# Kernel tuning notes

Measured on AMD Instinct MI355X. Metric: run time of the kernel, lower is better.

## Reference

```python
import jax, jax.numpy as jnp
import numpy as np

D = 1280      # embed_dim
H = 20        # num_heads
HD = D // H   # head_dim = 64
B = 4         # batch (number of requests)
ENC = 1500    # encoder length per request (Whisper 30s)
KV = B * ENC  # 6000 packed cross kv tokens
SEQ = [300, 500, 350, 450]  # ragged decoder lengths, sum = 1600
Q = sum(SEQ)


def setup_inputs() -> dict:
    key = jax.random.key(0)
    ks = jax.random.split(key, 8)
    s = 0.02
    return {
        "hidden_states": jax.random.normal(ks[0], (Q, D), jnp.float32),
        "cross_hidden_states": jax.random.normal(ks[1], (KV, D), jnp.float32),
        "seq_lens": jnp.array(SEQ, dtype=jnp.int32),
        "Wq": jax.random.normal(ks[2], (D, D), jnp.float32) * s,
        "bq": jax.random.normal(ks[3], (D,), jnp.float32) * s,
        "Wkv": jax.random.normal(ks[4], (D, 2 * D), jnp.float32) * s,
        "bkv": jax.random.normal(ks[5], (2 * D,), jnp.float32) * s,
        "Wo": jax.random.normal(ks[6], (D, D), jnp.float32) * s,
        "bo": jax.random.normal(ks[7], (D,), jnp.float32) * s,
    }


def reference(hidden_states, cross_hidden_states, seq_lens, Wq, bq, Wkv, bkv, Wo, bo):
    q_len, d = hidden_states.shape
    kv_len = cross_hidden_states.shape[0]
    bsz = seq_lens.shape[0]
    enc_len = kv_len // bsz
    scaling = jnp.float32(HD) ** -0.5

    # projections (packed tokens)
    q = (hidden_states @ Wq + bq) * scaling           # [Q, D]
    kv = cross_hidden_states @ Wkv + bkv              # [KV, 2D]
    k, v = kv[:, :d], kv[:, d:]

    # [H, L, HD]
    qh = q.reshape(q_len, H, HD).transpose(1, 0, 2)
    kh = k.reshape(kv_len, H, HD).transpose(1, 0, 2)
    vh = v.reshape(kv_len, H, HD).transpose(1, 0, 2)

    scores = jnp.einsum("hqd,hkd->hqk", qh, kh)       # [H, Q, KV]

    # ragged block-diagonal mask: query token i belongs to request
    # searchsorted(cumsum(seq_lens), i, 'right'); kv token j to j // enc_len
    cum = jnp.cumsum(seq_lens)
    q_req = jnp.searchsorted(cum, jnp.arange(q_len), side="right")
    kv_req = jnp.arange(kv_len) // enc_len
    mask = q_req[:, None] == kv_req[None, :]          # [Q, KV] bool

    scores = jnp.where(mask[None, :, :], scores, -jnp.inf)
    probs = jax.nn.softmax(scores, axis=-1)
    attn = jnp.einsum("hqk,hkd->hqd", probs, vh)      # [H, Q, HD]
    attn = attn.transpose(1, 0, 2).reshape(q_len, d)
    return attn @ Wo + bo
```

## Files before the change

kernel.cpp:

```cpp
#include <hip/hip_runtime.h>
#include <stdint.h>

#define AS1 __attribute__((address_space(1)))
#define AS3 __attribute__((address_space(3)))

typedef __bf16 bf16_t;
typedef bf16_t bf16x8 __attribute__((ext_vector_type(8)));
typedef float  f32x4  __attribute__((ext_vector_type(4)));
typedef float  f32x16 __attribute__((ext_vector_type(16)));
typedef unsigned short u16;

constexpr int D     = 1280;
constexpr int H     = 20;
constexpr int HD    = 64;
constexpr int NQ    = 1600;
constexpr int NKV   = 6000;
constexpr int ENC   = 1500;
constexpr int QPAD  = 1632;
constexpr int KVP   = 1504;
constexpr int KVTOT = 4 * KVP;
constexpr int KB_PER_REQ = KVP / 32;
constexpr int KB_TOT     = 4 * KB_PER_REQ;

__device__ __forceinline__ u16 f2bf(float f) {
  union { float f; uint32_t u; } x; x.f = f;
  uint32_t r = (x.u + 0x7fffu + ((x.u >> 16) & 1u)) >> 16;
  return (u16)r;
}

__device__ __forceinline__ void gload16(const void* g, void* l) {
  __builtin_amdgcn_global_load_lds((AS1 void*)g, (AS3 void*)l, 16, 0, 0);
}

__device__ __forceinline__ void cvt_body(const float* __restrict__ in, u16* __restrict__ out,
                                         int i, int n4) {
  if (i >= n4) return;
  float4 v = ((const float4*)in)[i];
  ushort4 o;
  o.x = f2bf(v.x); o.y = f2bf(v.y); o.z = f2bf(v.z); o.w = f2bf(v.w);
  ((ushort4*)out)[i] = o;
}

__device__ __forceinline__ void tpose_body(const float* __restrict__ in, u16* __restrict__ out,
                                           int R, int C, int bx, int by, u16 (*tile)[33]) {
  int bc = bx * 32, br = by * 32;
  int tx = threadIdx.x & 31, ty = threadIdx.x >> 5;
#pragma unroll
  for (int i = 0; i < 32; i += 8)
    tile[ty + i][tx] = f2bf(in[(size_t)(br + ty + i) * C + bc + tx]);
  __syncthreads();
#pragma unroll
  for (int i = 0; i < 32; i += 8)
    out[(size_t)(bc + ty + i) * R + br + tx] = tile[tx][ty + i];
}

__global__ __launch_bounds__(256)
void prep_kernel(const float* __restrict__ hs, const float* __restrict__ chs,
                 const float* __restrict__ Wq, const float* __restrict__ Wkv,
                 const float* __restrict__ Wo,
                 u16* __restrict__ hsb, u16* __restrict__ chsb,
                 u16* __restrict__ Wqt, u16* __restrict__ Wkvt, u16* __restrict__ Wot) {
  __shared__ u16 tile[32][33];
  int b = blockIdx.x;
  if (b < 2000) {
    cvt_body(hs, hsb, b * 256 + threadIdx.x, 512000);
  } else if (b < 9500) {
    cvt_body(chs, chsb, (b - 2000) * 256 + threadIdx.x, 1920000);
  } else if (b < 11100) {
    int t = b - 9500;  tpose_body(Wq,  Wqt,  1280, 1280, t % 40, t / 40, tile);
  } else if (b < 14300) {
    int t = b - 11100; tpose_body(Wkv, Wkvt, 1280, 2560, t % 80, t / 80, tile);
  } else {
    int t = b - 14300; tpose_body(Wo,  Wot,  1280, 1280, t % 40, t / 40, tile);
  }
}

template <int MODE>
__device__ __forceinline__ void gemm_tile(
    int m0, int n0, const u16* __restrict__ A, const u16* __restrict__ Bt,
    const float* __restrict__ bias, int M,
    u16* __restrict__ outA, u16* __restrict__ outB, float* __restrict__ outF,
    u16* As, u16* Bs) {
  const int tid = threadIdx.x;
  const int lane = tid & 63, l15 = lane & 15, lg = lane >> 4;
  const int w = tid >> 6, wr = w >> 1, wc = w & 1;

  const bool vside = (MODE == 1) && (n0 >= D);

  f32x4 acc[4][4] = {};

  for (int k0 = 0; k0 < D; k0 += 64) {
#pragma unroll
    for (int p = 0; p < 4; ++p) {
      int off = p * 4096 + tid * 16;
      int lg_off = off ^ (((off >> 7) & 7) << 4);
      int row = lg_off >> 7, kb = lg_off & 127;
      int gr = m0 + row; gr = gr < M ? gr : M - 1;
      gload16((const char*)A + ((size_t)gr * D + k0) * 2 + kb, (char*)As + off);
    }
#pragma unroll
    for (int p = 0; p < 4; ++p) {
      int off = p * 4096 + tid * 16;
      int lg_off = off ^ (((off >> 7) & 7) << 4);
      int row = lg_off >> 7, kb = lg_off & 127;
      int gr = n0 + row;
      gload16((const char*)Bt + ((size_t)gr * D + k0) * 2 + kb, (char*)Bs + off);
    }
    __syncthreads();
#pragma unroll
    for (int kk = 0; kk < 2; ++kk) {
      const int kbyte = kk * 64 + lg * 16;
      bf16x8 af[4], bfr[4];
#pragma unroll
      for (int m = 0; m < 4; ++m) {
        int row = wr * 64 + m * 16 + l15;
        int addr = ((row << 7) + kbyte) ^ ((row & 7) << 4);
        af[m] = *(const bf16x8*)((const char*)As + addr);
      }
#pragma unroll
      for (int n = 0; n < 4; ++n) {
        int row = wc * 64 + n * 16 + l15;
        int addr = ((row << 7) + kbyte) ^ ((row & 7) << 4);
        bfr[n] = *(const bf16x8*)((const char*)Bs + addr);
      }
      if (!vside) {
#pragma unroll
        for (int m = 0; m < 4; ++m)
#pragma unroll
          for (int n = 0; n < 4; ++n)
            acc[m][n] = __builtin_amdgcn_mfma_f32_16x16x32_bf16(af[m], bfr[n], acc[m][n], 0, 0, 0);
      } else {
#pragma unroll
        for (int m = 0; m < 4; ++m)
#pragma unroll
          for (int n = 0; n < 4; ++n)
            acc[m][n] = __builtin_amdgcn_mfma_f32_16x16x32_bf16(bfr[n], af[m], acc[m][n], 0, 0, 0);
      }
    }
    __syncthreads();
  }

  if (!vside) {
#pragma unroll
    for (int m = 0; m < 4; ++m)
#pragma unroll
      for (int n = 0; n < 4; ++n) {
        int col = n0 + wc * 64 + n * 16 + l15;
        float bv = bias[col];
#pragma unroll
        for (int r = 0; r < 4; ++r) {
          int row = m0 + wr * 64 + m * 16 + lg * 4 + r;
          if (row >= M) continue;
          float v = acc[m][n][r] + bv;
          if (MODE == 0) {
            v *= 0.125f;
            int h = col >> 6, hd = col & 63;
            outA[((size_t)(h * QPAD + row)) * HD + hd] = f2bf(v);
          } else if (MODE == 1) {
            int req = row / ENC, loc = row - req * ENC;
            int rr = req * KVP + loc;
            int h = col >> 6, hd = col & 63;
            int kb2 = rr >> 5, kv = rr & 31;
            outA[((size_t)((h * KB_TOT + kb2) * 4 + (hd >> 4))) * 512 + kv * 16 + (hd & 15)] = f2bf(v);
          } else {
            outF[(size_t)row * D + col] = v;
          }
        }
      }
  } else {
    float bvv[4][4];
#pragma unroll
    for (int n = 0; n < 4; ++n)
#pragma unroll
      for (int r = 0; r < 4; ++r)
        bvv[n][r] = bias[n0 + wc * 64 + n * 16 + lg * 4 + r];
#pragma unroll
    for (int m = 0; m < 4; ++m) {
      int gm = m0 + wr * 64 + m * 16 + l15;
      int req = gm / ENC, loc = gm - req * ENC;
      int rr = req * KVP + loc;
      int kb2 = rr >> 5, kv = rr & 31;
      bool ok = gm < M;
#pragma unroll
      for (int n = 0; n < 4; ++n)
#pragma unroll
        for (int r = 0; r < 4; ++r) {
          if (!ok) continue;
          int c2 = n0 + wc * 64 + n * 16 + lg * 4 + r - D;
          int h = c2 >> 6, hd = c2 & 63;
          outB[((size_t)((h * KB_TOT + kb2) * 64 + hd)) * 32 + kv] = f2bf(acc[m][n][r] + bvv[n][r]);
        }
    }
  }
}

__global__ __launch_bounds__(256)
void qkv_gemm_kernel(const u16* __restrict__ hsb, const u16* __restrict__ chsb,
                     const u16* __restrict__ Wqt, const u16* __restrict__ Wkvt,
                     const float* __restrict__ bq, const float* __restrict__ bkv,
                     u16* __restrict__ qhb, u16* __restrict__ khb, u16* __restrict__ vtb) {
  __shared__ __align__(16) u16 As[128 * 64];
  __shared__ __align__(16) u16 Bs[128 * 64];
  const int nwg = 1070, q8 = nwg >> 3, r8 = nwg & 7;
  const int xcd = blockIdx.x & 7, pos = blockIdx.x >> 3;
  const int wg = (xcd < r8 ? xcd * (q8 + 1) : r8 * (q8 + 1) + (xcd - r8) * q8) + pos;
  if (wg < 940) {
    gemm_tile<1>((wg / 20) * 128, (wg % 20) * 128, chsb, Wkvt, bkv, NKV,
                 khb, vtb, nullptr, As, Bs);
  } else {
    int w2 = wg - 940;
    gemm_tile<0>((w2 / 10) * 128, (w2 % 10) * 128, hsb, Wqt, bq, NQ,
                 qhb, nullptr, nullptr, As, Bs);
  }
}

__global__ __launch_bounds__(256)
void o_gemm_kernel(const u16* __restrict__ attnb, const u16* __restrict__ Wot,
                   const float* __restrict__ bo, float* __restrict__ out) {
  __shared__ __align__(16) u16 As[128 * 64];
  __shared__ __align__(16) u16 Bs[128 * 64];
  const int nwg = 130, q8 = nwg >> 3, r8 = nwg & 7;
  const int xcd = blockIdx.x & 7, pos = blockIdx.x >> 3;
  const int wg = (xcd < r8 ? xcd * (q8 + 1) : r8 * (q8 + 1) + (xcd - r8) * q8) + pos;
  gemm_tile<2>((wg / 10) * 128, (wg % 10) * 128, attnb, Wot, bo, NQ,
               nullptr, nullptr, out, As, Bs);
}

__global__ __launch_bounds__(256)
void attn_kernel(const u16* __restrict__ kbuf, const u16* __restrict__ vbuf,
                 const u16* __restrict__ qh, const int* __restrict__ seq,
                 u16* __restrict__ attnb) {
  __shared__ __align__(16) float smem[4][2176];
  const int lane = threadIdx.x & 63;
  const int l31 = lane & 31, h5 = lane >> 5;
  const int w = threadIdx.x >> 6;

  const int xcd = blockIdx.x & 7, pos = blockIdx.x >> 3;
  const int g = xcd * 160 + pos;
  const int p = g >> 4, t = g & 15;
  const int head = p >> 2, req = p & 3;

  int s0 = seq[0], s1 = seq[1], s2 = seq[2];
  int qstart = (req > 0 ? s0 : 0) + (req > 1 ? s1 : 0) + (req > 2 ? s2 : 0);
  int slen = seq[req];
  int q0 = t * 32;
  if (q0 >= slen) return;

  const u16* qrow = qh + ((size_t)(head * QPAD + qstart + q0 + l31)) * HD + h5 * 8;
  bf16x8 qb[4];
#pragma unroll
  for (int ks = 0; ks < 4; ++ks) qb[ks] = *(const bf16x8*)(qrow + ks * 16);

  const u16* kpan = kbuf + (size_t)(head * KB_TOT + req * KB_PER_REQ) * 2048 + l31 * 16 + h5 * 8;
  const u16* vpan = vbuf + (size_t)(head * KB_TOT + req * KB_PER_REQ) * 2048 + l31 * 32 + h5 * 8;
  const float C = 1.44269504088896340736f;

  f32x16 o0 = {}, o1 = {};
  float mx = -__builtin_inff(), ls = 0.f;

  const int kvs = w * 384;
  const int kve = (w == 3) ? ENC : kvs + 384;

  bf16x8 ka[4], va[2][2], kan[4], van[2][2];
  {
    const u16* kp = kpan + (size_t)(kvs >> 5) * 2048;
    const u16* vp = vpan + (size_t)(kvs >> 5) * 2048;
#pragma unroll
    for (int ks = 0; ks < 4; ++ks) ka[ks] = *(const bf16x8*)(kp + ks * 512);
#pragma unroll
    for (int dt = 0; dt < 2; ++dt)
#pragma unroll
      for (int ks = 0; ks < 2; ++ks)
        va[dt][ks] = *(const bf16x8*)(vp + dt * 1024 + ks * 16);
  }

  for (int kvb = kvs; kvb < kve; kvb += 32) {
    int nb = (kvb + 32 < kve ? kvb + 32 : kvs) >> 5;
    {
      const u16* kp = kpan + (size_t)nb * 2048;
      const u16* vp = vpan + (size_t)nb * 2048;
#pragma unroll
      for (int ks = 0; ks < 4; ++ks) kan[ks] = *(const bf16x8*)(kp + ks * 512);
#pragma unroll
      for (int dt = 0; dt < 2; ++dt)
#pragma unroll
        for (int ks = 0; ks < 2; ++ks)
          van[dt][ks] = *(const bf16x8*)(vp + dt * 1024 + ks * 16);
    }

    f32x16 sa = {};
    __builtin_amdgcn_s_setprio(1);
#pragma unroll
    for (int ks = 0; ks < 4; ++ks)
      sa = __builtin_amdgcn_mfma_f32_32x32x16_bf16(ka[ks], qb[ks], sa, 0, 0, 0);
    __builtin_amdgcn_s_setprio(0);

    if (kvb + 32 > ENC) {
#pragma unroll
      for (int r = 0; r < 16; ++r) {
        int kvr = (r & 3) + 4 * h5 + 8 * (r >> 2);
        sa[r] = (kvb + kvr >= ENC) ? -__builtin_inff() : sa[r];
      }
    }

    float tm = sa[0];
#pragma unroll
    for (int r = 1; r < 16; ++r) tm = fmaxf(tm, sa[r]);
    tm = fmaxf(tm, __shfl_xor(tm, 32));

    if (__any(tm > mx + 8.0f)) {
      float mnew = fmaxf(mx, tm);
      float sc = exp2f((mx - mnew) * C);
      mx = mnew;
      ls *= sc;
      o0 *= sc; o1 *= sc;
    }
    float psum = 0.f;
#pragma unroll
    for (int r = 0; r < 16; ++r) { sa[r] = exp2f((sa[r] - mx) * C); psum += sa[r]; }
    ls += psum;

    uint32_t a[8], x[8];
#pragma unroll
    for (int i = 0; i < 8; ++i)
      a[i] = (uint32_t)f2bf(sa[2 * i]) | ((uint32_t)f2bf(sa[2 * i + 1]) << 16);
#pragma unroll
    for (int i = 0; i < 8; ++i) x[i] = (uint32_t)__shfl_xor((int)a[i], 32);
    union { uint32_t w4[4]; bf16x8 v; } pb0, pb1;
    pb0.w4[0] = h5 ? x[2] : a[0]; pb0.w4[1] = h5 ? x[3] : a[1];
    pb0.w4[2] = h5 ? a[2] : x[0]; pb0.w4[3] = h5 ? a[3] : x[1];
    pb1.w4[0] = h5 ? x[6] : a[4]; pb1.w4[1] = h5 ? x[7] : a[5];
    pb1.w4[2] = h5 ? a[6] : x[4]; pb1.w4[3] = h5 ? a[7] : x[5];

    __builtin_amdgcn_s_setprio(1);
    o0 = __builtin_amdgcn_mfma_f32_32x32x16_bf16(va[0][0], pb0.v, o0, 0, 0, 0);
    o0 = __builtin_amdgcn_mfma_f32_32x32x16_bf16(va[0][1], pb1.v, o0, 0, 0, 0);
    o1 = __builtin_amdgcn_mfma_f32_32x32x16_bf16(va[1][0], pb0.v, o1, 0, 0, 0);
    o1 = __builtin_amdgcn_mfma_f32_32x32x16_bf16(va[1][1], pb1.v, o1, 0, 0, 0);
    __builtin_amdgcn_s_setprio(0);

#pragma unroll
    for (int ks = 0; ks < 4; ++ks) ka[ks] = kan[ks];
#pragma unroll
    for (int dt = 0; dt < 2; ++dt)
#pragma unroll
      for (int ks = 0; ks < 2; ++ks) va[dt][ks] = van[dt][ks];
  }

  ls += __shfl_xor(ls, 32);

#pragma unroll
  for (int r = 0; r < 16; ++r) {
    int drow = (r & 3) + 8 * (r >> 2) + 4 * h5;
    smem[w][drow * 33 + l31] = o0[r];
    smem[w][(drow + 32) * 33 + l31] = o1[r];
  }
  if (h5 == 0) {
    smem[w][2112 + l31] = mx;
    smem[w][2144 + l31] = ls;
  }
  __syncthreads();

#pragma unroll
  for (int it = 0; it < 8; ++it) {
    int item = threadIdx.x + it * 256;
    int q = item >> 6, d = item & 63;
    float m0v = smem[0][2112 + q], m1v = smem[1][2112 + q];
    float m2v = smem[2][2112 + q], m3v = smem[3][2112 + q];
    float M = fmaxf(fmaxf(m0v, m1v), fmaxf(m2v, m3v));
    float e0 = exp2f((m0v - M) * C), e1 = exp2f((m1v - M) * C);
    float e2 = exp2f((m2v - M) * C), e3 = exp2f((m3v - M) * C);
    float L = smem[0][2144 + q] * e0 + smem[1][2144 + q] * e1 +
              smem[2][2144 + q] * e2 + smem[3][2144 + q] * e3;
    float O = smem[0][d * 33 + q] * e0 + smem[1][d * 33 + q] * e1 +
              smem[2][d * 33 + q] * e2 + smem[3][d * 33 + q] * e3;
    int qr = q0 + q;
    if (qr < slen)
      attnb[(size_t)(qstart + qr) * D + head * HD + d] = f2bf(O / L);
  }
}

extern "C" void kernel_launch(void* const* d_in, const int* in_sizes, int n_in,
                              void* d_out, int out_size, void* d_ws, size_t ws_size,
                              hipStream_t stream) {
  const float* hs  = (const float*)d_in[0];
  const float* chs = (const float*)d_in[1];
  const int*   seq = (const int*)d_in[2];
  const float* Wq  = (const float*)d_in[3];
  const float* bq  = (const float*)d_in[4];
  const float* Wkv = (const float*)d_in[5];
  const float* bkv = (const float*)d_in[6];
  const float* Wo  = (const float*)d_in[7];
  const float* bo  = (const float*)d_in[8];

  char* ws = (char*)d_ws;
  u16* hsb   = (u16*)(ws + 0);
  u16* chsb  = (u16*)(ws + 4096000);
  u16* Wqt   = (u16*)(ws + 19456000);
  u16* Wkvt  = (u16*)(ws + 22732800);
  u16* Wot   = (u16*)(ws + 29286400);
  u16* qhb   = (u16*)(ws + 32563200);
  u16* khb   = (u16*)(ws + 36741120);
  u16* vtb   = (u16*)(ws + 52142080);
  u16* attnb = (u16*)(ws + 67543040);

  prep_kernel<<<15900, 256, 0, stream>>>(hs, chs, Wq, Wkv, Wo, hsb, chsb, Wqt, Wkvt, Wot);
  qkv_gemm_kernel<<<1070, 256, 0, stream>>>(hsb, chsb, Wqt, Wkvt, bq, bkv, qhb, khb, vtb);
  attn_kernel<<<1280, 256, 0, stream>>>(khb, vtb, qhb, seq, attnb);
  o_gemm_kernel<<<130, 256, 0, stream>>>(attnb, Wot, bo, (float*)d_out);
}
```

Measured before the change: 174.5 us.

## Double-buffer GEMM LDS tiles with two-stage prefetch interleaved into MFMA

Rewrites the shared GEMM tile loop to use two LDS buffers, prefetching the tile two steps ahead while MFMAs run on the current tile. Global-to-LDS loads are interleaved with MFMA groups, and fine-grained vmcnt waits plus raw barriers replace the full __syncthreads. It also raises the MFMA issue priority and adds a launch-bounds occupancy hint. The aim is to hide global load latency behind compute. In exchange it doubles LDS use to 64KB per block, which limits occupancy, and it depends on exact waitcnt accounting being correct.

```diff
diff --git a/kernel.cpp b/kernel.cpp
--- a/kernel.cpp
+++ b/kernel.cpp
@@ -80,64 +80,80 @@
     int m0, int n0, const u16* __restrict__ A, const u16* __restrict__ Bt,
     const float* __restrict__ bias, int M,
     u16* __restrict__ outA, u16* __restrict__ outB, float* __restrict__ outF,
-    u16* As, u16* Bs) {
+    u16* lds) {
   const int tid = threadIdx.x;
   const int lane = tid & 63, l15 = lane & 15, lg = lane >> 4;
   const int w = tid >> 6, wr = w >> 1, wc = w & 1;
-
   const bool vside = (MODE == 1) && (n0 >= D);
+  constexpr int NT = D / 64;
+
+  auto stage = [&](int tj, int c) {
+    int buf = (tj & 1) * 32768;
+    if (c < 4) {
+      int off = c * 4096 + tid * 16;
+      int loff = off ^ (((off >> 7) & 7) << 4);
+      int row = loff >> 7, colb = loff & 127;
+      int gr = m0 + row; gr = gr < M ? gr : M - 1;
+      gload16((const char*)A + ((size_t)gr * D + tj * 64) * 2 + colb,
+              (char*)lds + buf + off);
+    } else {
+      int off = (c - 4) * 4096 + tid * 16;
+      int loff = off ^ (((off >> 7) & 7) << 4);
+      int row = loff >> 7, colb = loff & 127;
+      int gr = n0 + row;
+      gload16((const char*)Bt + ((size_t)gr * D + tj * 64) * 2 + colb,
+              (char*)lds + buf + 16384 + off);
+    }
+  };
 
   f32x4 acc[4][4] = {};
 
-  for (int k0 = 0; k0 < D; k0 += 64) {
-#pragma unroll
-    for (int p = 0; p < 4; ++p) {
-      int off = p * 4096 + tid * 16;
-      int lg_off = off ^ (((off >> 7) & 7) << 4);
-      int row = lg_off >> 7, kb = lg_off & 127;
-      int gr = m0 + row; gr = gr < M ? gr : M - 1;
-      gload16((const char*)A + ((size_t)gr * D + k0) * 2 + kb, (char*)As + off);
-    }
-#pragma unroll
-    for (int p = 0; p < 4; ++p) {
-      int off = p * 4096 + tid * 16;
-      int lg_off = off ^ (((off >> 7) & 7) << 4);
-      int row = lg_off >> 7, kb = lg_off & 127;
-      int gr = n0 + row;
-      gload16((const char*)Bt + ((size_t)gr * D + k0) * 2 + kb, (char*)Bs + off);
-    }
-    __syncthreads();
-#pragma unroll
-    for (int kk = 0; kk < 2; ++kk) {
-      const int kbyte = kk * 64 + lg * 16;
-      bf16x8 af[4], bfr[4];
-#pragma unroll
-      for (int m = 0; m < 4; ++m) {
+#pragma unroll
+  for (int c = 0; c < 8; ++c) stage(0, c);
+#pragma unroll
+  for (int c = 0; c < 8; ++c) stage(1, c);
+  asm volatile("s_waitcnt vmcnt(8)" ::: "memory");
+  __builtin_amdgcn_s_barrier();
+
+  for (int t = 0; t < NT; ++t) {
+    const char* base = (const char*)lds + (t & 1) * 32768;
+    bf16x8 af[4][2], bfr[4][2];
+#pragma unroll
+    for (int m = 0; m < 4; ++m)
+#pragma unroll
+      for (int kh = 0; kh < 2; ++kh) {
         int row = wr * 64 + m * 16 + l15;
-        int addr = ((row << 7) + kbyte) ^ ((row & 7) << 4);
-        af[m] = *(const bf16x8*)((const char*)As + addr);
+        int bo = (row << 7) + kh * 64 + lg * 16;
+        af[m][kh] = *(const bf16x8*)(base + (bo ^ ((row & 7) << 4)));
       }
 #pragma unroll
-      for (int n = 0; n < 4; ++n) {
+    for (int n = 0; n < 4; ++n)
+#pragma unroll
+      for (int kh = 0; kh < 2; ++kh) {
         int row = wc * 64 + n * 16 + l15;
-        int addr = ((row << 7) + kbyte) ^ ((row & 7) << 4);
-        bfr[n] = *(const bf16x8*)((const char*)Bs + addr);
+        int bo = (row << 7) + kh * 64 + lg * 16;
+        bfr[n][kh] = *(const bf16x8*)(base + 16384 + (bo ^ ((row & 7) << 4)));
       }
-      if (!vside) {
-#pragma unroll
-        for (int m = 0; m < 4; ++m)
-#pragma unroll
-          for (int n = 0; n < 4; ++n)
-            acc[m][n] = __builtin_amdgcn_mfma_f32_16x16x32_bf16(af[m], bfr[n], acc[m][n], 0, 0, 0);
-      } else {
-#pragma unroll
-        for (int m = 0; m < 4; ++m)
-#pragma unroll
-          for (int n = 0; n < 4; ++n)
-            acc[m][n] = __builtin_amdgcn_mfma_f32_16x16x32_bf16(bfr[n], af[m], acc[m][n], 0, 0, 0);
-      }
-    }
-    __syncthreads();
+    asm volatile("s_waitcnt lgkmcnt(0)" ::: "memory");
+    __builtin_amdgcn_s_barrier();
+
+    int pt = t + 2;
+#pragma unroll
+    for (int c = 0; c < 4; ++c) {
+      if (pt < NT) { stage(pt, 2 * c); stage(pt, 2 * c + 1); }
+      __builtin_amdgcn_s_setprio(1);
+#pragma unroll
+      for (int m = 0; m < 4; ++m)
+#pragma unroll
+        for (int kh = 0; kh < 2; ++kh)
+          acc[m][c] = vside
+            ? __builtin_amdgcn_mfma_f32_16x16x32_bf16(bfr[c][kh], af[m][kh], acc[m][c], 0, 0, 0)
+            : __builtin_amdgcn_mfma_f32_16x16x32_bf16(af[m][kh], bfr[c][kh], acc[m][c], 0, 0, 0);
+      __builtin_amdgcn_s_setprio(0);
+    }
+    if (t < NT - 2)       asm volatile("s_waitcnt vmcnt(8)" ::: "memory");
+    else if (t == NT - 2) asm volatile("s_waitcnt vmcnt(0)" ::: "memory");
+    if (t < NT - 1) __builtin_amdgcn_s_barrier();
   }
 
   if (!vside) {
@@ -194,36 +210,34 @@
   }
 }
 
-__global__ __launch_bounds__(256)
+__global__ __launch_bounds__(256, 2)
 void qkv_gemm_kernel(const u16* __restrict__ hsb, const u16* __restrict__ chsb,
                      const u16* __restrict__ Wqt, const u16* __restrict__ Wkvt,
                      const float* __restrict__ bq, const float* __restrict__ bkv,
                      u16* __restrict__ qhb, u16* __restrict__ khb, u16* __restrict__ vtb) {
-  __shared__ __align__(16) u16 As[128 * 64];
-  __shared__ __align__(16) u16 Bs[128 * 64];
+  __shared__ __align__(16) u16 lds[32768];
   const int nwg = 1070, q8 = nwg >> 3, r8 = nwg & 7;
   const int xcd = blockIdx.x & 7, pos = blockIdx.x >> 3;
   const int wg = (xcd < r8 ? xcd * (q8 + 1) : r8 * (q8 + 1) + (xcd - r8) * q8) + pos;
   if (wg < 940) {
     gemm_tile<1>((wg / 20) * 128, (wg % 20) * 128, chsb, Wkvt, bkv, NKV,
-                 khb, vtb, nullptr, As, Bs);
+                 khb, vtb, nullptr, lds);
   } else {
     int w2 = wg - 940;
     gemm_tile<0>((w2 / 10) * 128, (w2 % 10) * 128, hsb, Wqt, bq, NQ,
-                 qhb, nullptr, nullptr, As, Bs);
-  }
-}
-
-__global__ __launch_bounds__(256)
+                 qhb, nullptr, nullptr, lds);
+  }
+}
+
+__global__ __launch_bounds__(256, 2)
 void o_gemm_kernel(const u16* __restrict__ attnb, const u16* __restrict__ Wot,
                    const float* __restrict__ bo, float* __restrict__ out) {
-  __shared__ __align__(16) u16 As[128 * 64];
-  __shared__ __align__(16) u16 Bs[128 * 64];
+  __shared__ __align__(16) u16 lds[32768];
   const int nwg = 130, q8 = nwg >> 3, r8 = nwg & 7;
   const int xcd = blockIdx.x & 7, pos = blockIdx.x >> 3;
   const int wg = (xcd < r8 ? xcd * (q8 + 1) : r8 * (q8 + 1) + (xcd - r8) * q8) + pos;
   gemm_tile<2>((wg / 10) * 128, (wg % 10) * 128, attnb, Wot, bo, NQ,
-               nullptr, nullptr, out, As, Bs);
+               nullptr, nullptr, out, lds);
 }
 
 __global__ __launch_bounds__(256)
```

Result: faster. 167.6 us (-4.0%).
